# Performance work log

Hardware: AMD Instinct MI355X
Metric: run time of the kernel (lower is better)

Reference implementation:

```python
import jax, jax.numpy as jnp
import numpy as np

TP, TQ, B = 600, 60, 64          # passage len, question len, batch
H, H2, EMB = 256, 128, 344       # hidden, hidden//2, embed(300)+pos_tags(44)


def _lstm_cell(x, h, c, Wih, Whh, b):
    # PyTorch nn.LSTMCell math; b = b_ih + b_hh, gate order i,f,g,o
    g = x @ Wih.T + h @ Whh.T + b
    i, f, gg, o = jnp.split(g, 4, axis=-1)
    c2 = jax.nn.sigmoid(f) * c + jax.nn.sigmoid(i) * jnp.tanh(gg)
    return jax.nn.sigmoid(o) * jnp.tanh(c2), c2


def _pre_bilstm(x, mask, Wih, Whh, b):
    # Faithful quirk of the source: the cell's h output is DISCARDED;
    # c is masked and h = tanh(c).
    Bb = x.shape[1]
    init = (jnp.zeros((Bb, H2), x.dtype), jnp.zeros((Bb, H2), x.dtype))

    def step(carry, inp):
        h, c = carry
        xt, mt = inp
        _, c2 = _lstm_cell(xt, h, c, Wih, Whh, b)
        c2 = c2 * mt
        h2 = jnp.tanh(c2)
        return (h2, c2), h2

    _, Hf = jax.lax.scan(step, init, (x, mask))
    _, Hb = jax.lax.scan(step, init, (x[::-1], mask[::-1]))
    return jnp.concatenate([Hf, Hb[::-1]], axis=-1)  # [T,B,H]


def _match(Hp, Hq, mask, Wq, Wp, bp, Wh, Wa, ba, Wih, Whh, b):
    aq = Hq @ Wq.T           # [TQ,B,H] attend_question_for_passage (no bias)
    ap = Hp @ Wp.T + bp      # [TP,B,H] attend_passage_for_passage (precomputed)
    Bb = Hp.shape[1]
    init = (jnp.zeros((Bb, H2), Hp.dtype), jnp.zeros((Bb, H2), Hp.dtype))

    def step(carry, inp):
        h, c = carry
        apt, hpt, mt = inp
        g = jnp.tanh(aq + apt + h @ Wh.T)               # [TQ,B,H]
        alpha = jax.nn.softmax(g @ Wa.T + ba, axis=0)   # softmax over TQ, [TQ,B,1]
        wHq = jnp.einsum('tbo,tbh->bh', alpha, Hq)      # weighted question
        z = jnp.concatenate([hpt, wHq], axis=-1)        # [B,2H]
        h2, c2 = _lstm_cell(z, h, c, Wih, Whh, b)
        h2, c2 = h2 * mt, c2 * mt                       # mask applied to h and c
        return (h2, c2), h2

    _, Hf = jax.lax.scan(step, init, (ap, Hp, mask))
    _, Hb = jax.lax.scan(step, init, (ap[::-1], Hp[::-1], mask[::-1]))
    return jnp.concatenate([Hf, Hb[::-1]], axis=-1)  # [TP,B,H]


def setup_inputs() -> dict:
    key = jax.random.key(0)
    ks = iter(jax.random.split(key, 32))

    def w(shape, s=0.08):
        return jax.random.normal(next(ks), shape, jnp.float32) * s

    return {
        "passage": jax.random.normal(next(ks), (TP, B, EMB), jnp.float32),
        "question": jax.random.normal(next(ks), (TQ, B, EMB), jnp.float32),
        "mask_p": jnp.ones((TP, B, 1), jnp.float32),
        "mask_q": jnp.ones((TQ, B, 1), jnp.float32),
        "pre0_Wih": w((4 * H2, EMB)), "pre0_Whh": w((4 * H2, H2)), "pre0_b": w((4 * H2,)),
        "pre1_Wih": w((4 * H2, H)), "pre1_Whh": w((4 * H2, H2)), "pre1_b": w((4 * H2,)),
        "mq_Wq": w((H, H)), "mq_Wp": w((H, H)), "mq_bp": w((H,)),
        "mq_Wh": w((H, H2)), "mq_Wa": w((1, H)), "mq_ba": w((1,)),
        "mq_Wih": w((4 * H2, 2 * H)), "mq_Whh": w((4 * H2, H2)), "mq_b": w((4 * H2,)),
    }


def reference(passage, question, mask_p, mask_q,
              pre0_Wih, pre0_Whh, pre0_b,
              pre1_Wih, pre1_Whh, pre1_b,
              mq_Wq, mq_Wp, mq_bp, mq_Wh, mq_Wa, mq_ba,
              mq_Wih, mq_Whh, mq_b):
    # preprocessing layer 0 (shared LSTM for passage and question), dropout=0 eval
    Hp = _pre_bilstm(passage, mask_p, pre0_Wih, pre0_Whh, pre0_b)
    Hq = _pre_bilstm(question, mask_q, pre0_Wih, pre0_Whh, pre0_b)
    # preprocessing layer 1
    Hp = _pre_bilstm(Hp, mask_p, pre1_Wih, pre1_Whh, pre1_b)
    Hq = _pre_bilstm(Hq, mask_q, pre1_Wih, pre1_Whh, pre1_b)
    # passage Match-LSTM layer (bidirectional, question-attention per step)
    Hr = _match(Hp, Hq, mask_p, mq_Wq, mq_Wp, mq_bp, mq_Wh, mq_Wa, mq_ba,
                mq_Wih, mq_Whh, mq_b)
    return Hr  # [TP, B, H]
```

## Files before the change

kernel.cpp:

```cpp
#include <hip/hip_runtime.h>

typedef unsigned int u32;
typedef _Float16 f16x2 __attribute__((ext_vector_type(2)));

#define TP 600
#define TQ 60
#define BB 64
#define EMB 344
#define HH 256
#define H2 128
#define GG 512

__device__ __forceinline__ float exp2_fast(float x){
#if __has_builtin(__builtin_amdgcn_exp2f)
    return __builtin_amdgcn_exp2f(x);
#else
    return exp2f(x);
#endif
}
__device__ __forceinline__ float rcp_fast(float x){
#if __has_builtin(__builtin_amdgcn_rcpf)
    return __builtin_amdgcn_rcpf(x);
#else
    return 1.0f / x;
#endif
}
__device__ __forceinline__ float sigm_fast(float x){
    return rcp_fast(1.f + exp2_fast(-1.44269504f * x));
}
__device__ __forceinline__ float tanh_fast(float x){
    return 1.f - 2.f * rcp_fast(1.f + exp2_fast(2.88539008f * x));
}
__device__ __forceinline__ float dot2x(u32 w, u32 h, float acc){
    f16x2 wv = __builtin_bit_cast(f16x2, w);
    f16x2 hv = __builtin_bit_cast(f16x2, h);
    acc = fmaf((float)wv.x, (float)hv.x, acc);
    acc = fmaf((float)wv.y, (float)hv.y, acc);
    return acc;
}
__device__ __forceinline__ float dot2f(u32 w, u32 h, float acc){
#if __has_builtin(__builtin_amdgcn_fdot2)
    return __builtin_amdgcn_fdot2(__builtin_bit_cast(f16x2, w),
                                  __builtin_bit_cast(f16x2, h), acc, false);
#else
    return dot2x(w, h, acc);
#endif
}
__device__ __forceinline__ u32 pack2(float a, float b){
    f16x2 v; v.x = (_Float16)a; v.y = (_Float16)b;
    return __builtin_bit_cast(u32, v);
}
__device__ __forceinline__ u32 lane_bcast(u32 v, int l){
    return (u32)__builtin_amdgcn_readlane((int)v, l);
}

__global__ void prep_kernel(const float* __restrict__ pre0_Wih, const float* __restrict__ pre0_Whh,
                            const float* __restrict__ pre1_Wih, const float* __restrict__ pre1_Whh,
                            const float* __restrict__ Wq, const float* __restrict__ Wp,
                            const float* __restrict__ Whm,
                            const float* __restrict__ Whhm,
                            float* __restrict__ WT0, float* __restrict__ WT1,
                            float* __restrict__ WTq, float* __restrict__ WTp,
                            float* __restrict__ WTz, const float* __restrict__ Wihm,
                            u32* __restrict__ P0hh, u32* __restrict__ P1hh,
                            u32* __restrict__ PMhh, u32* __restrict__ PMwh)
{
    int g = blockIdx.x * blockDim.x + threadIdx.x;
    int gs = gridDim.x * blockDim.x;
    for (int idx = g; idx < 512*344; idx += gs) {
        int j = idx / 344, k = idx - j*344;
        WT0[((k>>2)*512 + j)*4 + (k&3)] = pre0_Wih[idx];
    }
    for (int idx = g; idx < 512*256; idx += gs) {
        int j = idx >> 8, k = idx & 255;
        WT1[((k>>2)*512 + j)*4 + (k&3)] = pre1_Wih[idx];
    }
    for (int idx = g; idx < 256*256; idx += gs) {
        int j = idx >> 8, k = idx & 255;
        WTq[((k>>2)*256 + j)*4 + (k&3)] = Wq[idx];
        WTp[((k>>2)*256 + j)*4 + (k&3)] = Wp[idx];
    }
    for (int idx = g; idx < 512*256; idx += gs) {
        int j = idx >> 8, k = idx & 255;
        WTz[((k>>2)*512 + j)*4 + (k&3)] = Wihm[j*512 + k];
    }
    for (int idx = g; idx < 64*512; idx += gs) {
        int k2 = idx >> 9, j = idx & 511;
        P0hh[idx] = pack2(pre0_Whh[j*128 + 2*k2], pre0_Whh[j*128 + 2*k2 + 1]);
        P1hh[idx] = pack2(pre1_Whh[j*128 + 2*k2], pre1_Whh[j*128 + 2*k2 + 1]);
        PMhh[idx] = pack2(Whhm[j*128 + 2*k2], Whhm[j*128 + 2*k2 + 1]);
    }
    for (int idx = g; idx < 64*256; idx += gs) {
        int k2 = idx >> 8, j = idx & 255;
        PMwh[idx] = pack2(Whm[j*128 + 2*k2], Whm[j*128 + 2*k2 + 1]);
    }
}

template<int K, int M>
__global__ __launch_bounds__(M)
void proj_kernel(const float* __restrict__ X0, const float* __restrict__ W0,
                 const float* __restrict__ b0, float* __restrict__ C0, int T0,
                 const float* __restrict__ X1, const float* __restrict__ W1,
                 const float* __restrict__ b1, float* __restrict__ C1)
{
    __shared__ float Xs[K*68];
    int t = blockIdx.x;
    const float* X; const float* W; const float* bias; float* C; int trow;
    if (t < T0) { X = X0; W = W0; bias = b0; C = C0; trow = t; }
    else        { X = X1; W = W1; bias = b1; C = C1; trow = t - T0; }
    int j = threadIdx.x;
    for (int b = 0; b < 64; ++b) {
        for (int k = j; k < K; k += M)
            Xs[k*68 + b] = X[(trow*64 + b)*K + k];
    }
    __syncthreads();
    float acc[64];
    float binit = bias ? bias[j] : 0.f;
    #pragma unroll
    for (int b = 0; b < 64; ++b) acc[b] = binit;
    const float4* W4 = (const float4*)W;
    for (int k4 = 0; k4 < K/4; ++k4) {
        float4 w4 = W4[k4*M + j];
        float wv[4] = {w4.x, w4.y, w4.z, w4.w};
        #pragma unroll
        for (int kk = 0; kk < 4; ++kk) {
            int k = 4*k4 + kk;
            #pragma unroll
            for (int b4 = 0; b4 < 16; ++b4) {
                float4 x4 = *((const float4*)&Xs[k*68 + 4*b4]);
                acc[4*b4+0] = fmaf(wv[kk], x4.x, acc[4*b4+0]);
                acc[4*b4+1] = fmaf(wv[kk], x4.y, acc[4*b4+1]);
                acc[4*b4+2] = fmaf(wv[kk], x4.z, acc[4*b4+2]);
                acc[4*b4+3] = fmaf(wv[kk], x4.w, acc[4*b4+3]);
            }
        }
    }
    for (int b = 0; b < 64; ++b)
        C[(trow*64 + b)*M + j] = acc[b];
}

__global__ __launch_bounds__(512)
void yq_kernel(const float* __restrict__ Hq1, const float* __restrict__ Wihm,
               float* __restrict__ Yq)
{
    __shared__ float Xs[256*68];
    int tq = blockIdx.x;
    int j = threadIdx.x;
    for (int b = 0; b < 64; ++b) {
        for (int k = j; k < 256; k += 512)
            Xs[k*68 + b] = Hq1[(tq*64 + b)*256 + k];
    }
    __syncthreads();
    float acc[64];
    #pragma unroll
    for (int b = 0; b < 64; ++b) acc[b] = 0.f;
    const float4* W4 = (const float4*)(Wihm + j*512 + 256);
    for (int k4 = 0; k4 < 64; ++k4) {
        float4 w4 = W4[k4];
        float wv[4] = {w4.x, w4.y, w4.z, w4.w};
        #pragma unroll
        for (int kk = 0; kk < 4; ++kk) {
            int k = 4*k4 + kk;
            #pragma unroll
            for (int b4 = 0; b4 < 16; ++b4) {
                float4 x4 = *((const float4*)&Xs[k*68 + 4*b4]);
                acc[4*b4+0] = fmaf(wv[kk], x4.x, acc[4*b4+0]);
                acc[4*b4+1] = fmaf(wv[kk], x4.y, acc[4*b4+1]);
                acc[4*b4+2] = fmaf(wv[kk], x4.z, acc[4*b4+2]);
                acc[4*b4+3] = fmaf(wv[kk], x4.w, acc[4*b4+3]);
            }
        }
    }
    for (int b = 0; b < 64; ++b)
        Yq[(tq*64 + b)*512 + j] = acc[b];
}

__global__ __launch_bounds__(384)
void rec_pre_kernel(const float* __restrict__ Xp, const float* __restrict__ Xq,
                    const u32* __restrict__ Whh,
                    const float* __restrict__ mask_p, const float* __restrict__ mask_q,
                    float* __restrict__ Hp, float* __restrict__ Hq)
{
    int bid = blockIdx.x;
    int sub = bid & 127; int b = sub >> 1; int dir = sub & 1;
    const float* X; const float* mask; float* Hout; int T;
    if (bid < 128) { X = Xp; mask = mask_p; Hout = Hp; T = TP; }
    else           { X = Xq; mask = mask_q; Hout = Hq; T = TQ; }
    int j = threadIdx.x;
    __shared__ __align__(16) _Float16 h16[128];
    __shared__ float gates[384];
    u32 w[64];
    #pragma unroll
    for (int q = 0; q < 64; ++q) w[q] = Whh[q*512 + j];
    if (j < 128) h16[j] = (_Float16)0.f;
    float c = 0.f;
    int ti0 = dir ? (T-1) : 0;
    float x_c = X[(ti0*64 + b)*512 + j];
    float m_c = mask[ti0*64 + b];
    int cls = j >> 7;
    __syncthreads();
    const u32* h32 = (const u32*)h16;
    for (int s = 0; s < T; ++s) {
        int ti = dir ? (T-1-s) : s;
        int s1 = (s+1 < T) ? (s+1) : s;
        int tn = dir ? (T-1-s1) : s1;
        float x_n = X[(tn*64 + b)*512 + j];
        float m_n = mask[tn*64 + b];
        u32 hp = h32[j & 63];
        float a0 = x_c, a1 = 0.f, a2 = 0.f, a3 = 0.f;
        #pragma unroll
        for (int q = 0; q < 64; q += 4) {
            u32 h0 = lane_bcast(hp, q),   h1 = lane_bcast(hp, q+1);
            u32 h2v = lane_bcast(hp, q+2), h3 = lane_bcast(hp, q+3);
            a0 = dot2f(w[q],   h0,  a0);
            a1 = dot2f(w[q+1], h1,  a1);
            a2 = dot2f(w[q+2], h2v, a2);
            a3 = dot2f(w[q+3], h3,  a3);
        }
        float g = (a0 + a1) + (a2 + a3);
        gates[j] = (cls == 2) ? tanh_fast(g) : sigm_fast(g);
        __syncthreads();
        if (j < 128) {
            float gi = gates[j], gf = gates[128+j], gg = gates[256+j];
            c = gf*c + gi*gg;
            c *= m_c;
            float h = tanh_fast(c);
            h16[j] = (_Float16)h;
            Hout[(ti*64 + b)*256 + dir*128 + j] = h;
        }
        __syncthreads();
        x_c = x_n; m_c = m_n;
    }
}

__global__ __launch_bounds__(512)
__attribute__((amdgpu_waves_per_eu(2, 2)))
void match_kernel(const float* __restrict__ ap,
                  const float* __restrict__ aqg,
                  const float* __restrict__ Zp,
                  const float* __restrict__ Yq,
                  const float* __restrict__ Wa,
                  const float* __restrict__ mask_p,
                  const u32* __restrict__ PMwh,
                  const u32* __restrict__ PMhh,
                  float* __restrict__ out)
{
    int bid = blockIdx.x; int b = bid >> 1; int dir = bid & 1;
    int tid = threadIdx.x;
    __shared__ __align__(16) u32 sumt16[160];
    __shared__ float gates[512];
    __shared__ __align__(16) _Float16 h16[128];
    __shared__ __align__(16) _Float16 e16[64];

    int tq = tid >> 3, sb = tid & 7;

    u32 aqr[16];
    if (tq < 60) {
        #pragma unroll
        for (int i = 0; i < 16; ++i) {
            float2 a = *(const float2*)&aqg[(tq*64 + b)*256 + 32*sb + 2*i];
            aqr[i] = pack2(a.x, a.y);
        }
    } else {
        #pragma unroll
        for (int i = 0; i < 16; ++i) aqr[i] = 0u;
    }
    u32 wa_reg[16];
    #pragma unroll
    for (int i = 0; i < 16; ++i) {
        float2 w2 = *(const float2*)&Wa[32*sb + 2*i];
        wa_reg[i] = pack2(w2.x, w2.y);
    }
    u32 Yqr[32];
    #pragma unroll
    for (int r = 0; r < 30; ++r) {
        float y0 = Yq[((2*r  )*64 + b)*512 + tid];
        float y1 = Yq[((2*r+1)*64 + b)*512 + tid];
        Yqr[r] = pack2(y0, y1);
    }
    Yqr[30] = 0u; Yqr[31] = 0u;
    u32 whh[64];
    #pragma unroll
    for (int q = 0; q < 64; ++q) whh[q] = PMhh[q*512 + tid];
    u32 wh[64];
    {
        int jw = tid & 255;
        #pragma unroll
        for (int q = 0; q < 64; ++q) wh[q] = PMwh[q*256 + jw];
    }
    if (tid < 128) h16[tid] = (_Float16)0.f;

    float c = 0.f;
    int ti0 = dir ? (TP-1) : 0;
    float zp_c = Zp[(ti0*64 + b)*512 + tid];
    float ap_c = (tid < 256) ? ap[(ti0*64 + b)*256 + tid] : 0.f;
    float m_c  = mask_p[ti0*64 + b];
    int cls = tid >> 7;
    const u32 ONE2 = 0x3C003C00u;
    float h_out = 0.f; int ti_prev = 0;
    __syncthreads();

    const u32* h32 = (const u32*)h16;
    const u32* e32 = (const u32*)e16;

    for (int s = 0; s < TP; ++s) {
        int ti = dir ? (TP-1-s) : s;
        int s1 = (s+1 < TP) ? (s+1) : s;
        int tn = dir ? (TP-1-s1) : s1;

        if (s && tid < 128)
            out[(ti_prev*64 + b)*256 + dir*128 + tid] = h_out;
        float zp_n = Zp[(tn*64 + b)*512 + tid];
        float ap_n = (tid < 256) ? ap[(tn*64 + b)*256 + tid] : 0.f;
        float m_n  = mask_p[tn*64 + b];

        u32 hp = h32[tid & 63];
        float w0 = 0.f, w1 = 0.f, w2a = 0.f, w3a = 0.f;
        if (tid < 256) {
            float s0 = ap_c, s1a = 0.f, s2 = 0.f, s3 = 0.f;
            #pragma unroll
            for (int q = 0; q < 64; q += 4) {
                u32 h0 = lane_bcast(hp, q),   u1 = lane_bcast(hp, q+1);
                u32 h2v = lane_bcast(hp, q+2), h3 = lane_bcast(hp, q+3);
                w0  = dot2f(whh[q],   h0,  w0);  s0  = dot2f(wh[q],   h0,  s0);
                w1  = dot2f(whh[q+1], u1,  w1);  s1a = dot2f(wh[q+1], u1,  s1a);
                w2a = dot2f(whh[q+2], h2v, w2a); s2  = dot2f(wh[q+2], h2v, s2);
                w3a = dot2f(whh[q+3], h3,  w3a); s3  = dot2f(wh[q+3], h3,  s3);
            }
            float st = (s0 + s1a) + (s2 + s3);
            float so = __shfl_xor(st, 1);
            if ((tid & 1) == 0) {
                int p = tid >> 1;
                sumt16[(p >> 4)*20 + (p & 15)] = pack2(st, so);
            }
        } else {
            #pragma unroll
            for (int q = 0; q < 64; q += 4) {
                u32 h0 = lane_bcast(hp, q),   u1 = lane_bcast(hp, q+1);
                u32 h2v = lane_bcast(hp, q+2), h3 = lane_bcast(hp, q+3);
                w0  = dot2f(whh[q],   h0,  w0);
                w1  = dot2f(whh[q+1], u1,  w1);
                w2a = dot2f(whh[q+2], h2v, w2a);
                w3a = dot2f(whh[q+3], h3,  w3a);
            }
        }
        float hwhh = (w0 + w1) + (w2a + w3a);
        __syncthreads();

        {
            const uint4* sv4 = (const uint4*)&sumt16[sb*20];
            uint4 sv0 = sv4[0], sv1 = sv4[1], sv2 = sv4[2], sv3 = sv4[3];
            u32 sa[16] = {sv0.x,sv0.y,sv0.z,sv0.w, sv1.x,sv1.y,sv1.z,sv1.w,
                          sv2.x,sv2.y,sv2.z,sv2.w, sv3.x,sv3.y,sv3.z,sv3.w};
            float p0 = 0.f, p1 = 0.f, p2 = 0.f, p3 = 0.f;
            #pragma unroll
            for (int i = 0; i < 16; ++i) {
                f16x2 sm = __builtin_bit_cast(f16x2, aqr[i]) +
                           __builtin_bit_cast(f16x2, sa[i]);
                f16x2 wv = __builtin_bit_cast(f16x2, wa_reg[i]);
                float t0 = tanh_fast((float)sm.x);
                float t1 = tanh_fast((float)sm.y);
                if (i & 1) { p2 = fmaf((float)wv.x, t0, p2); p3 = fmaf((float)wv.y, t1, p3); }
                else       { p0 = fmaf((float)wv.x, t0, p0); p1 = fmaf((float)wv.y, t1, p1); }
            }
            float part = (p0 + p1) + (p2 + p3);
            part += __shfl_xor(part, 1);
            part += __shfl_xor(part, 2);
            part += __shfl_xor(part, 4);
            float sc = fminf(9.f, fmaxf(-9.f, part));
            float e = exp2_fast(sc * 1.44269504f);
            if (tq >= 60) e = 0.f;
            if (sb == 0) e16[tq] = (_Float16)e;
        }
        __syncthreads();

        {
            u32 ep = e32[tid & 31];
            float y0 = 0.f, y1 = 0.f, S0 = 0.f, S1 = 0.f;
            #pragma unroll
            for (int r4 = 0; r4 < 8; ++r4) {
                u32 e0 = lane_bcast(ep, 4*r4+0), e1 = lane_bcast(ep, 4*r4+1);
                u32 e2 = lane_bcast(ep, 4*r4+2), e3 = lane_bcast(ep, 4*r4+3);
                y0 = dot2f(Yqr[4*r4+0], e0, y0); S0 = dot2f(ONE2, e0, S0);
                y1 = dot2f(Yqr[4*r4+1], e1, y1); S1 = dot2f(ONE2, e1, S1);
                y0 = dot2f(Yqr[4*r4+2], e2, y0); S0 = dot2f(ONE2, e2, S0);
                y1 = dot2f(Yqr[4*r4+3], e3, y1); S1 = dot2f(ONE2, e3, S1);
            }
            float rn = rcp_fast(S0 + S1);
            float g = zp_c + rn * (y0 + y1) + hwhh;
            gates[tid] = (cls == 2) ? tanh_fast(g) : sigm_fast(g);
        }
        __syncthreads();

        if (tid < 128) {
            float gi = gates[tid], gf = gates[128+tid], gg = gates[256+tid], go = gates[384+tid];
            c = gf*c + gi*gg;
            float h = go * tanh_fast(c);
            h *= m_c; c *= m_c;
            h16[tid] = (_Float16)h;
            h_out = h; ti_prev = ti;
        }
        __syncthreads();
        zp_c = zp_n; ap_c = ap_n; m_c = m_n;
    }
    if (tid < 128)
        out[(ti_prev*64 + b)*256 + dir*128 + tid] = h_out;
}

#define O_BUFX   0UL
#define O_BUFXQ  19660800UL
#define O_HP0    21626880UL
#define O_HQ0    31457280UL
#define O_HP1    32440320UL
#define O_HQ1    42270720UL
#define O_WT0    43253760UL
#define O_WT1    43429888UL
#define O_WTQ    43560960UL
#define O_WTP    43626496UL
#define O_WTZ    43692032UL
#define O_P0HH   43823104UL
#define O_P1HH   43855872UL
#define O_PMHH   43888640UL
#define O_PMWH   43921408UL

extern "C" void kernel_launch(void* const* d_in, const int* in_sizes, int n_in,
                              void* d_out, int out_size, void* d_ws, size_t ws_size,
                              hipStream_t stream)
{
    const float* passage  = (const float*)d_in[0];
    const float* question = (const float*)d_in[1];
    const float* mask_p   = (const float*)d_in[2];
    const float* mask_q   = (const float*)d_in[3];
    const float* pre0_Wih = (const float*)d_in[4];
    const float* pre0_Whh = (const float*)d_in[5];
    const float* pre0_b   = (const float*)d_in[6];
    const float* pre1_Wih = (const float*)d_in[7];
    const float* pre1_Whh = (const float*)d_in[8];
    const float* pre1_b   = (const float*)d_in[9];
    const float* mq_Wq    = (const float*)d_in[10];
    const float* mq_Wp    = (const float*)d_in[11];
    const float* mq_bp    = (const float*)d_in[12];
    const float* mq_Wh    = (const float*)d_in[13];
    const float* mq_Wa    = (const float*)d_in[14];
    const float* mq_Wih   = (const float*)d_in[16];
    const float* mq_Whh   = (const float*)d_in[17];
    const float* mq_b     = (const float*)d_in[18];

    float* ws = (float*)d_ws;
    float* bufX  = ws + O_BUFX;
    float* bufXq = ws + O_BUFXQ;
    float* Hp0   = ws + O_HP0;
    float* Hq0   = ws + O_HQ0;
    float* Hp1   = ws + O_HP1;
    float* Hq1   = ws + O_HQ1;
    float* WT0   = ws + O_WT0;
    float* WT1   = ws + O_WT1;
    float* WTq   = ws + O_WTQ;
    float* WTp   = ws + O_WTP;
    float* WTz   = ws + O_WTZ;
    u32*   P0hh  = (u32*)(ws + O_P0HH);
    u32*   P1hh  = (u32*)(ws + O_P1HH);
    u32*   PMhh  = (u32*)(ws + O_PMHH);
    u32*   PMwh  = (u32*)(ws + O_PMWH);
    float* ap = Hp0;
    float* aq = Hq0;
    float* Zp = bufX;
    float* Yq = bufXq;

    prep_kernel<<<688, 256, 0, stream>>>(pre0_Wih, pre0_Whh, pre1_Wih, pre1_Whh,
                                         mq_Wq, mq_Wp, mq_Wh, mq_Whh,
                                         WT0, WT1, WTq, WTp, WTz, mq_Wih,
                                         P0hh, P1hh, PMhh, PMwh);
    proj_kernel<EMB, 512><<<660, 512, 0, stream>>>(passage, WT0, pre0_b, bufX, TP,
                                                   question, WT0, pre0_b, bufXq);
    rec_pre_kernel<<<256, 384, 0, stream>>>(bufX, bufXq, P0hh, mask_p, mask_q, Hp0, Hq0);
    proj_kernel<256, 512><<<660, 512, 0, stream>>>(Hp0, WT1, pre1_b, bufX, TP,
                                                   Hq0, WT1, pre1_b, bufXq);
    rec_pre_kernel<<<256, 384, 0, stream>>>(bufX, bufXq, P1hh, mask_p, mask_q, Hp1, Hq1);
    proj_kernel<256, 256><<<660, 256, 0, stream>>>(Hp1, WTp, mq_bp, ap, TP,
                                                   Hq1, WTq, nullptr, aq);
    proj_kernel<256, 512><<<600, 512, 0, stream>>>(Hp1, WTz, mq_b, Zp, TP,
                                                   nullptr, nullptr, nullptr, nullptr);
    yq_kernel<<<60, 512, 0, stream>>>(Hq1, mq_Wih, Yq);
    match_kernel<<<128, 512, 0, stream>>>(ap, aq, Zp, Yq, mq_Wa, mask_p,
                                          PMwh, PMhh, (float*)d_out);
}
```

Baseline: 3.742 ms.

## Fuse LSTM gate computation per thread and cut barriers in recurrent kernels

Measured after the change: 3.820 ms. 2.1% more time.

```diff
diff --git a/kernel.cpp b/kernel.cpp
--- a/kernel.cpp
+++ b/kernel.cpp
@@ -52,6 +52,9 @@
 }
 __device__ __forceinline__ u32 lane_bcast(u32 v, int l){
     return (u32)__builtin_amdgcn_readlane((int)v, l);
+}
+__device__ __forceinline__ void bar_lds(){
+    asm volatile("s_waitcnt lgkmcnt(0)\n\ts_barrier" ::: "memory");
 }
 
 __global__ void prep_kernel(const float* __restrict__ pre0_Wih, const float* __restrict__ pre0_Whh,
@@ -175,7 +178,8 @@
         Yq[(tq*64 + b)*512 + j] = acc[b];
 }
 
-__global__ __launch_bounds__(384)
+__global__ __launch_bounds__(128)
+__attribute__((amdgpu_waves_per_eu(1, 1)))
 void rec_pre_kernel(const float* __restrict__ Xp, const float* __restrict__ Xq,
                     const u32* __restrict__ Whh,
                     const float* __restrict__ mask_p, const float* __restrict__ mask_q,
@@ -187,49 +191,52 @@
     if (bid < 128) { X = Xp; mask = mask_p; Hout = Hp; T = TP; }
     else           { X = Xq; mask = mask_q; Hout = Hq; T = TQ; }
     int j = threadIdx.x;
-    __shared__ __align__(16) _Float16 h16[128];
-    __shared__ float gates[384];
-    u32 w[64];
-    #pragma unroll
-    for (int q = 0; q < 64; ++q) w[q] = Whh[q*512 + j];
-    if (j < 128) h16[j] = (_Float16)0.f;
+    int l = j & 63;
+    __shared__ __align__(8) _Float16 hbuf[2][128];
+    u32 wi[64], wf[64], wg[64];
+    #pragma unroll
+    for (int q = 0; q < 64; ++q) {
+        wi[q] = Whh[q*512 +       j];
+        wf[q] = Whh[q*512 + 128 + j];
+        wg[q] = Whh[q*512 + 256 + j];
+    }
+    hbuf[0][j] = (_Float16)0.f;
     float c = 0.f;
-    int ti0 = dir ? (T-1) : 0;
-    float x_c = X[(ti0*64 + b)*512 + j];
-    float m_c = mask[ti0*64 + b];
-    int cls = j >> 7;
-    __syncthreads();
-    const u32* h32 = (const u32*)h16;
+    int t0 = dir ? (T-1) : 0;
+    int t1i = (T > 1) ? (dir ? (T-2) : 1) : t0;
+    float xi0 = X[(t0*64+b)*512 + j],       xf0 = X[(t0*64+b)*512 + 128 + j],
+          xg0 = X[(t0*64+b)*512 + 256 + j], m0  = mask[t0*64+b];
+    float xi1 = X[(t1i*64+b)*512 + j],       xf1 = X[(t1i*64+b)*512 + 128 + j],
+          xg1 = X[(t1i*64+b)*512 + 256 + j], m1  = mask[t1i*64+b];
+    bar_lds();
+    int buf = 0;
+    const u32* hb32 = (const u32*)hbuf;
     for (int s = 0; s < T; ++s) {
         int ti = dir ? (T-1-s) : s;
-        int s1 = (s+1 < T) ? (s+1) : s;
-        int tn = dir ? (T-1-s1) : s1;
-        float x_n = X[(tn*64 + b)*512 + j];
-        float m_n = mask[tn*64 + b];
-        u32 hp = h32[j & 63];
-        float a0 = x_c, a1 = 0.f, a2 = 0.f, a3 = 0.f;
-        #pragma unroll
-        for (int q = 0; q < 64; q += 4) {
-            u32 h0 = lane_bcast(hp, q),   h1 = lane_bcast(hp, q+1);
-            u32 h2v = lane_bcast(hp, q+2), h3 = lane_bcast(hp, q+3);
-            a0 = dot2f(w[q],   h0,  a0);
-            a1 = dot2f(w[q+1], h1,  a1);
-            a2 = dot2f(w[q+2], h2v, a2);
-            a3 = dot2f(w[q+3], h3,  a3);
-        }
-        float g = (a0 + a1) + (a2 + a3);
-        gates[j] = (cls == 2) ? tanh_fast(g) : sigm_fast(g);
-        __syncthreads();
-        if (j < 128) {
-            float gi = gates[j], gf = gates[128+j], gg = gates[256+j];
-            c = gf*c + gi*gg;
-            c *= m_c;
-            float h = tanh_fast(c);
-            h16[j] = (_Float16)h;
-            Hout[(ti*64 + b)*256 + dir*128 + j] = h;
-        }
-        __syncthreads();
-        x_c = x_n; m_c = m_n;
+        int s2 = (s+2 < T) ? (s+2) : (T-1);
+        int t2 = dir ? (T-1-s2) : s2;
+        float xi2 = X[(t2*64+b)*512 + j],       xf2 = X[(t2*64+b)*512 + 128 + j],
+              xg2 = X[(t2*64+b)*512 + 256 + j], m2  = mask[t2*64+b];
+        u32 hp = hb32[buf*64 + l];
+        float ai0 = xi0, ai1 = 0.f, af0 = xf0, af1 = 0.f, ag0 = xg0, ag1 = 0.f;
+        #pragma unroll
+        for (int q = 0; q < 64; q += 2) {
+            u32 h0 = lane_bcast(hp, q), h1 = lane_bcast(hp, q+1);
+            ai0 = dot2f(wi[q],   h0, ai0); af0 = dot2f(wf[q],   h0, af0); ag0 = dot2f(wg[q],   h0, ag0);
+            ai1 = dot2f(wi[q+1], h1, ai1); af1 = dot2f(wf[q+1], h1, af1); ag1 = dot2f(wg[q+1], h1, ag1);
+        }
+        float gi = sigm_fast(ai0 + ai1);
+        float gf = sigm_fast(af0 + af1);
+        float gg = tanh_fast(ag0 + ag1);
+        c = gf*c + gi*gg;
+        c *= m0;
+        float h = tanh_fast(c);
+        hbuf[buf^1][j] = (_Float16)h;
+        Hout[(ti*64 + b)*256 + dir*128 + j] = h;
+        bar_lds();
+        buf ^= 1;
+        xi0=xi1; xf0=xf1; xg0=xg1; m0=m1;
+        xi1=xi2; xf1=xf2; xg1=xg2; m1=m2;
     }
 }
 
@@ -248,11 +255,10 @@
     int bid = blockIdx.x; int b = bid >> 1; int dir = bid & 1;
     int tid = threadIdx.x;
     __shared__ __align__(16) u32 sumt16[160];
-    __shared__ float gates[512];
-    __shared__ __align__(16) _Float16 h16[128];
+    __shared__ __align__(16) float gates[512];
     __shared__ __align__(16) _Float16 e16[64];
 
-    int tq = tid >> 3, sb = tid & 7;
+    int tq = tid >> 3, sb = tid & 7, l = tid & 63;
 
     u32 aqr[16];
     if (tq < 60) {
@@ -288,19 +294,18 @@
         #pragma unroll
         for (int q = 0; q < 64; ++q) wh[q] = PMwh[q*256 + jw];
     }
-    if (tid < 128) h16[tid] = (_Float16)0.f;
-
-    float c = 0.f;
+
+    float c0 = 0.f, c1 = 0.f;
+    u32 hp = 0u;
     int ti0 = dir ? (TP-1) : 0;
     float zp_c = Zp[(ti0*64 + b)*512 + tid];
     float ap_c = (tid < 256) ? ap[(ti0*64 + b)*256 + tid] : 0.f;
     float m_c  = mask_p[ti0*64 + b];
     int cls = tid >> 7;
     const u32 ONE2 = 0x3C003C00u;
-    float h_out = 0.f; int ti_prev = 0;
-    __syncthreads();
-
-    const u32* h32 = (const u32*)h16;
+    float h_out0 = 0.f, h_out1 = 0.f; int ti_prev = 0;
+    bar_lds();
+
     const u32* e32 = (const u32*)e16;
 
     for (int s = 0; s < TP; ++s) {
@@ -308,13 +313,6 @@
         int s1 = (s+1 < TP) ? (s+1) : s;
         int tn = dir ? (TP-1-s1) : s1;
 
-        if (s && tid < 128)
-            out[(ti_prev*64 + b)*256 + dir*128 + tid] = h_out;
-        float zp_n = Zp[(tn*64 + b)*512 + tid];
-        float ap_n = (tid < 256) ? ap[(tn*64 + b)*256 + tid] : 0.f;
-        float m_n  = mask_p[tn*64 + b];
-
-        u32 hp = h32[tid & 63];
         float w0 = 0.f, w1 = 0.f, w2a = 0.f, w3a = 0.f;
         if (tid < 256) {
             float s0 = ap_c, s1a = 0.f, s2 = 0.f, s3 = 0.f;
@@ -345,7 +343,15 @@
             }
         }
         float hwhh = (w0 + w1) + (w2a + w3a);
-        __syncthreads();
+        bar_lds();
+
+        if (s && tid < 64) {
+            float2 hv; hv.x = h_out0; hv.y = h_out1;
+            *(float2*)&out[(ti_prev*64 + b)*256 + dir*128 + 2*l] = hv;
+        }
+        float zp_n = Zp[(tn*64 + b)*512 + tid];
+        float ap_n = (tid < 256) ? ap[(tn*64 + b)*256 + tid] : 0.f;
+        float m_n  = mask_p[tn*64 + b];
 
         {
             const uint4* sv4 = (const uint4*)&sumt16[sb*20];
@@ -372,10 +378,10 @@
             if (tq >= 60) e = 0.f;
             if (sb == 0) e16[tq] = (_Float16)e;
         }
-        __syncthreads();
+        bar_lds();
 
         {
-            u32 ep = e32[tid & 31];
+            u32 ep = e32[l & 31];
             float y0 = 0.f, y1 = 0.f, S0 = 0.f, S1 = 0.f;
             #pragma unroll
             for (int r4 = 0; r4 < 8; ++r4) {
@@ -390,21 +396,27 @@
             float g = zp_c + rn * (y0 + y1) + hwhh;
             gates[tid] = (cls == 2) ? tanh_fast(g) : sigm_fast(g);
         }
-        __syncthreads();
-
-        if (tid < 128) {
-            float gi = gates[tid], gf = gates[128+tid], gg = gates[256+tid], go = gates[384+tid];
-            c = gf*c + gi*gg;
-            float h = go * tanh_fast(c);
-            h *= m_c; c *= m_c;
-            h16[tid] = (_Float16)h;
-            h_out = h; ti_prev = ti;
-        }
-        __syncthreads();
+        bar_lds();
+
+        {
+            float2 gi2 = *(const float2*)&gates[      2*l];
+            float2 gf2 = *(const float2*)&gates[128 + 2*l];
+            float2 gg2 = *(const float2*)&gates[256 + 2*l];
+            float2 go2 = *(const float2*)&gates[384 + 2*l];
+            c0 = gf2.x*c0 + gi2.x*gg2.x;
+            c1 = gf2.y*c1 + gi2.y*gg2.y;
+            float h0 = go2.x * tanh_fast(c0);
+            float h1 = go2.y * tanh_fast(c1);
+            h0 *= m_c; h1 *= m_c; c0 *= m_c; c1 *= m_c;
+            hp = pack2(h0, h1);
+            h_out0 = h0; h_out1 = h1; ti_prev = ti;
+        }
         zp_c = zp_n; ap_c = ap_n; m_c = m_n;
     }
-    if (tid < 128)
-        out[(ti_prev*64 + b)*256 + dir*128 + tid] = h_out;
+    if (tid < 64) {
+        float2 hv; hv.x = h_out0; hv.y = h_out1;
+        *(float2*)&out[(ti_prev*64 + b)*256 + dir*128 + 2*l] = hv;
+    }
 }
 
 #define O_BUFX   0UL
@@ -473,10 +485,10 @@
                                          P0hh, P1hh, PMhh, PMwh);
     proj_kernel<EMB, 512><<<660, 512, 0, stream>>>(passage, WT0, pre0_b, bufX, TP,
                                                    question, WT0, pre0_b, bufXq);
-    rec_pre_kernel<<<256, 384, 0, stream>>>(bufX, bufXq, P0hh, mask_p, mask_q, Hp0, Hq0);
+    rec_pre_kernel<<<256, 128, 0, stream>>>(bufX, bufXq, P0hh, mask_p, mask_q, Hp0, Hq0);
     proj_kernel<256, 512><<<660, 512, 0, stream>>>(Hp0, WT1, pre1_b, bufX, TP,
                                                    Hq0, WT1, pre1_b, bufXq);
-    rec_pre_kernel<<<256, 384, 0, stream>>>(bufX, bufXq, P1hh, mask_p, mask_q, Hp1, Hq1);
+    rec_pre_kernel<<<256, 128, 0, stream>>>(bufX, bufXq, P1hh, mask_p, mask_q, Hp1, Hq1);
     proj_kernel<256, 256><<<660, 256, 0, stream>>>(Hp1, WTp, mq_bp, ap, TP,
                                                    Hq1, WTq, nullptr, aq);
     proj_kernel<256, 512><<<600, 512, 0, stream>>>(Hp1, WTz, mq_b, Zp, TP,
```
